# Performance work log

Measured on AMD Instinct MI355X. Metric: run time of the kernel, lower is better.

The kernel has to match this reference:

```python
import jax, jax.numpy as jnp
import numpy as np

# icosphere level-6 mesh dims
B, CIN, COUT = 8, 64, 64
NV_PREV, NV, NF = 10242, 40962, 81920


def spmm(x, rows, cols, vals, nrows):
    # x: [..., ncols]; sparse S [nrows, ncols] in COO -> y[..., r] = sum S[r,c] x[..., c]
    out = jnp.zeros(x.shape[:-1] + (nrows,), x.dtype)
    return out.at[..., rows].add(x[..., cols] * vals)


def setup_inputs() -> dict:
    key = jax.random.key(0)
    ks = jax.random.split(key, 12)
    x = jax.random.normal(ks[0], (B, CIN, NV_PREV), jnp.float32)
    # G: per-face gradient operator [3*NF, NV], 3 nnz per row (face vertices)
    G_rows = jnp.repeat(jnp.arange(3 * NF, dtype=jnp.int32), 3)
    G_cols = jax.random.randint(ks[1], (3 * NF * 3,), 0, NV, dtype=jnp.int32)
    G_vals = jax.random.normal(ks[2], (3 * NF * 3,), jnp.float32) * 0.1
    # L: vertex Laplacian [NV, NV], ~7 nnz per row
    L_rows = jnp.repeat(jnp.arange(NV, dtype=jnp.int32), 7)
    L_cols = jax.random.randint(ks[3], (NV * 7,), 0, NV, dtype=jnp.int32)
    L_vals = jax.random.normal(ks[4], (NV * 7,), jnp.float32) * 0.1
    # F2V: face-to-vertex averaging [NV, NF], ~6 nnz per row
    F2V_rows = jnp.repeat(jnp.arange(NV, dtype=jnp.int32), 6)
    F2V_cols = jax.random.randint(ks[5], (NV * 6,), 0, NF, dtype=jnp.int32)
    F2V_vals = jnp.full((NV * 6,), 1.0 / 6.0, jnp.float32)
    # per-face east-west / north-south tangent weights [NF, 3]
    EW = jax.random.normal(ks[6], (NF, 3), jnp.float32)
    NS = jax.random.normal(ks[7], (NF, 3), jnp.float32)
    # learned parameters
    stdv = 1.0 / np.sqrt(CIN * 4)
    coeffs = jax.random.uniform(ks[8], (COUT, CIN, 4), jnp.float32, -stdv, stdv)
    bias = jax.random.uniform(ks[9], (COUT,), jnp.float32, -stdv, stdv)
    return {
        "x": x,
        "G_rows": G_rows, "G_cols": G_cols, "G_vals": G_vals,
        "L_rows": L_rows, "L_cols": L_cols, "L_vals": L_vals,
        "F2V_rows": F2V_rows, "F2V_cols": F2V_cols, "F2V_vals": F2V_vals,
        "EW": EW, "NS": NS, "coeffs": coeffs, "bias": bias,
    }


def reference(x, G_rows, G_cols, G_vals, L_rows, L_cols, L_vals,
              F2V_rows, F2V_cols, F2V_vals, EW, NS, coeffs, bias):
    b, c = x.shape[:2]
    # pad new (upsampled) vertices with ones: [B, C, NV]
    xin = jnp.concatenate([x, jnp.ones((b, c, NV - NV_PREV), x.dtype)], axis=-1)
    # per-face gradient: [B, C, 3*NF] -> [B, C, NF, 3]
    grad_face = spmm(xin, G_rows, G_cols, G_vals, 3 * NF)
    grad_face = grad_face.reshape(b, c, 3, NF).transpose(0, 1, 3, 2)
    # Laplacian: [B, C, NV]
    laplacian = spmm(xin, L_rows, L_cols, L_vals, NV)
    # project face gradients onto EW/NS tangent dirs: [B, C, NF]
    grad_face_ew = jnp.sum(grad_face * EW, axis=-1)
    grad_face_ns = jnp.sum(grad_face * NS, axis=-1)
    # average back to vertices: [B, C, NV]
    grad_vert_ew = spmm(grad_face_ew, F2V_rows, F2V_cols, F2V_vals, NV)
    grad_vert_ns = spmm(grad_face_ns, F2V_rows, F2V_cols, F2V_vals, NV)
    # fuse 4 feature maps with learned coeffs: [B, CIN, NV, 4] x [COUT, CIN, 4]
    feat = jnp.stack([xin, laplacian, grad_vert_ew, grad_vert_ns], axis=-1)
    out = jnp.einsum("bcvk,ock->bov", feat, coeffs) + bias[:, None]
    return out
```

## Files before the change

kernel.cpp:

```cpp
#include <hip/hip_runtime.h>
#include <hip/hip_bf16.h>

typedef __hip_bfloat16 bf16;
typedef __attribute__((ext_vector_type(8))) short short8;
typedef __attribute__((ext_vector_type(4))) float floatx4;

#define NVP 10242
#define NV  40962
#define NF  81920
#define VPB 32
#define FPW 4

__device__ __forceinline__ float bfbits2f(unsigned short u) {
    union { unsigned int i; float f; } cv; cv.i = ((unsigned int)u) << 16;
    return cv.f;
}
__device__ __forceinline__ unsigned short f2bfbits(float f) {
    bf16 h = __float2bfloat16(f);
    return __builtin_bit_cast(unsigned short, h);
}
__device__ __forceinline__ unsigned short pk_fp8(float a, float b) {
    int p = __builtin_amdgcn_cvt_pk_fp8_f32(a, b, 0, false);
    return (unsigned short)(p & 0xffff);
}
__device__ __forceinline__ unsigned char one_fp8(float a) {
    int p = __builtin_amdgcn_cvt_pk_fp8_f32(a, 0.f, 0, false);
    return (unsigned char)(p & 0xff);
}
__device__ __forceinline__ float fp8_lo(unsigned int u) {
    return __builtin_amdgcn_cvt_f32_fp8(u, 0);
}
__device__ __forceinline__ float fp8_hi(unsigned int u) {
    return __builtin_amdgcn_cvt_f32_fp8(u, 1);
}

__global__ void k_prep(const float* __restrict__ coeffs,
                       unsigned short* __restrict__ coeffsB,
                       const int* __restrict__ G_cols,
                       const float* __restrict__ G_vals,
                       const float* __restrict__ EW,
                       const float* __restrict__ NS,
                       float* __restrict__ Gpk,
                       const int* __restrict__ L_cols,
                       const float* __restrict__ L_vals,
                       const int* __restrict__ F2V_cols,
                       const float* __restrict__ F2V_vals,
                       float* __restrict__ Vpk) {
    int b = blockIdx.x;
    if (b < 64) {
        int t = b * 256 + threadIdx.x;
        int j = t & 7, lane = (t >> 3) & 63, s = t >> 9;
        int ot = s >> 3, kk = s & 7;
        int o  = ot * 16 + (lane & 15);
        int kg = kk * 32 + (lane >> 4) * 8 + j;
        coeffsB[t] = f2bfbits(coeffs[o * 256 + kg]);
    } else if (b < 384) {
        int f = (b - 64) * 256 + threadIdx.x;
        float r[32];
#pragma unroll
        for (int q = 0; q < 32; ++q) r[q] = 0.f;
#pragma unroll
        for (int d = 0; d < 3; ++d)
#pragma unroll
            for (int j = 0; j < 3; ++j) {
                int idx = (d * NF + f) * 3 + j;
                r[d * 3 + j]      = __int_as_float(G_cols[idx]);
                r[16 + d * 3 + j] = G_vals[idx];
            }
#pragma unroll
        for (int d = 0; d < 3; ++d) {
            r[25 + d] = EW[f * 3 + d];
            r[28 + d] = NS[f * 3 + d];
        }
        float4* dst = (float4*)(Gpk + (size_t)f * 32);
#pragma unroll
        for (int q = 0; q < 8; ++q) dst[q] = ((const float4*)r)[q];
    } else {
        int v = (b - 384) * 256 + threadIdx.x;
        if (v >= NV) return;
        float r[32];
#pragma unroll
        for (int q = 0; q < 32; ++q) r[q] = 0.f;
#pragma unroll
        for (int j = 0; j < 7; ++j) {
            r[j]      = __int_as_float(L_cols[v * 7 + j]);
            r[16 + j] = L_vals[v * 7 + j];
        }
#pragma unroll
        for (int j = 0; j < 6; ++j) {
            r[8 + j]  = __int_as_float(F2V_cols[v * 6 + j]);
            r[24 + j] = F2V_vals[v * 6 + j];
        }
        float4* dst = (float4*)(Vpk + (size_t)v * 32);
#pragma unroll
        for (int q = 0; q < 8; ++q) dst[q] = ((const float4*)r)[q];
    }
}

__global__ void k_transpose(const float* __restrict__ x,
                            unsigned short* __restrict__ xin,
                            unsigned char* __restrict__ xin8) {
    x    += (size_t)blockIdx.y * 64 * NVP;
    xin  += (size_t)blockIdx.y * 64 * NV;
    xin8 += (size_t)blockIdx.y * 64 * NV;
    __shared__ float tile[64][65];
    int v0 = blockIdx.x * 64;
    int tx = threadIdx.x & 63;
    int ty = threadIdx.x >> 6;
    int v  = v0 + tx;
#pragma unroll
    for (int r = 0; r < 16; ++r) {
        int c = ty + r * 4;
        tile[tx][c] = (v < NVP) ? x[c * NVP + v] : 1.0f;
    }
    __syncthreads();
#pragma unroll
    for (int r = 0; r < 16; ++r) {
        int vl = ty + r * 4;
        int vv = v0 + vl;
        if (vv < NV) {
            float val = tile[vl][tx];
            xin [vv * 64 + tx] = f2bfbits(val);
            xin8[vv * 64 + tx] = one_fp8(val);
        }
    }
}

__global__ void __launch_bounds__(256, 4) k_facegrad(
    const unsigned char* __restrict__ xin8,
    const float* __restrict__ Gpk,
    unsigned short* __restrict__ gfi, int nbm, int nbs) {
    int batch = blockIdx.x & nbm;
    int fblk  = blockIdx.x >> nbs;
    xin8 += (size_t)batch * 64 * NV;
    gfi  += (size_t)batch * 64 * NF;
    int w  = __builtin_amdgcn_readfirstlane(threadIdx.x >> 6);
    int c  = threadIdx.x & 63;
    int f0 = (fblk * 4 + w) * FPW;

    int gc[FPW][9];
#pragma unroll
    for (int i = 0; i < FPW; ++i) {
        const int* ri = (const int*)(Gpk + (size_t)(f0 + i) * 32);
#pragma unroll
        for (int j = 0; j < 9; ++j) gc[i][j] = ri[j];
    }
    unsigned int xv[FPW][9];
#pragma unroll
    for (int i = 0; i < FPW; ++i)
#pragma unroll
        for (int j = 0; j < 9; ++j)
            xv[i][j] = xin8[(size_t)gc[i][j] * 64 + c];
#pragma unroll
    for (int i = 0; i < FPW; ++i) {
        const float* rf = Gpk + (size_t)(f0 + i) * 32;
        float g0 = rf[16] * fp8_lo(xv[i][0]) + rf[17] * fp8_lo(xv[i][1])
                 + rf[18] * fp8_lo(xv[i][2]);
        float g1 = rf[19] * fp8_lo(xv[i][3]) + rf[20] * fp8_lo(xv[i][4])
                 + rf[21] * fp8_lo(xv[i][5]);
        float g2 = rf[22] * fp8_lo(xv[i][6]) + rf[23] * fp8_lo(xv[i][7])
                 + rf[24] * fp8_lo(xv[i][8]);
        float ew = g0 * rf[25] + g1 * rf[26] + g2 * rf[27];
        float ns = g0 * rf[28] + g1 * rf[29] + g2 * rf[30];
        gfi[(f0 + i) * 64 + c] = pk_fp8(ew, ns);
    }
}

__global__ void __launch_bounds__(512, 2) k_vertex(
    const unsigned short* __restrict__ xin,
    const unsigned char* __restrict__ xin8,
    const float* __restrict__ Vpk,
    const unsigned short* __restrict__ gfi,
    const unsigned short* __restrict__ coeffsB,
    const float* __restrict__ bias,
    float* __restrict__ out,
    int nbm, int nbs) {
    int batch = blockIdx.x & nbm;
    int vb    = (blockIdx.x >> nbs) * VPB;
    xin  += (size_t)batch * 64 * NV;
    xin8 += (size_t)batch * 64 * NV;
    gfi  += (size_t)batch * 64 * NF;
    out  += (size_t)batch * 64 * NV;

    __shared__ unsigned short feat[VPB * 264];
    __shared__ float outs[VPB * 65];
    int w    = __builtin_amdgcn_readfirstlane(threadIdx.x >> 6);
    int lane = threadIdx.x & 63;
    int c    = lane;

    int vcs[4];
#pragma unroll
    for (int i = 0; i < 4; ++i) {
        int v = vb + w * 4 + i;
        vcs[i] = __builtin_amdgcn_readfirstlane(v < NV ? v : NV - 1);
    }
    int lc[4][7], fc[4][6];
#pragma unroll
    for (int i = 0; i < 4; ++i) {
        const int* ri = (const int*)(Vpk + (size_t)vcs[i] * 32);
#pragma unroll
        for (int j = 0; j < 7; ++j) lc[i][j] = ri[j];
#pragma unroll
        for (int j = 0; j < 6; ++j) fc[i][j] = ri[8 + j];
    }
    unsigned int f0u[4], xl[4][7], gg[4][6];
#pragma unroll
    for (int i = 0; i < 4; ++i) {
        f0u[i] = xin[(size_t)vcs[i] * 64 + c];
#pragma unroll
        for (int j = 0; j < 7; ++j)
            xl[i][j] = xin8[(size_t)lc[i][j] * 64 + c];
#pragma unroll
        for (int j = 0; j < 6; ++j)
            gg[i][j] = gfi[(size_t)fc[i][j] * 64 + c];
    }
#pragma unroll
    for (int i = 0; i < 4; ++i) {
        const float* rv = Vpk + (size_t)vcs[i] * 32;
        float lap = 0.f;
#pragma unroll
        for (int j = 0; j < 7; ++j)
            lap += rv[16 + j] * fp8_lo(xl[i][j]);
        float ew = 0.f, ns = 0.f;
#pragma unroll
        for (int j = 0; j < 6; ++j) {
            float val = rv[24 + j];
            ew += val * fp8_lo(gg[i][j]);
            ns += val * fp8_hi(gg[i][j]);
        }
        ushort4 p = make_ushort4((unsigned short)f0u[i], f2bfbits(lap),
                                 f2bfbits(ew), f2bfbits(ns));
        *(ushort4*)&feat[(w * 4 + i) * 264 + c * 4] = p;
    }
    __syncthreads();

    int m = lane & 15, quad = lane >> 4;
    int ot = w & 3, vh = w >> 2;
    float bo = bias[ot * 16 + m];
    floatx4 acc = {bo, bo, bo, bo};
#pragma unroll
    for (int kk = 0; kk < 8; ++kk) {
        short8 a = *(const short8*)&feat[(vh * 16 + m) * 264 + kk * 32 + quad * 8];
        short8 bfr = *(const short8*)&coeffsB[((ot * 8 + kk) * 64 + lane) * 8];
        acc = __builtin_amdgcn_mfma_f32_16x16x32_bf16(a, bfr, acc, 0, 0, 0);
    }

#pragma unroll
    for (int r = 0; r < 4; ++r)
        outs[(vh * 16 + quad * 4 + r) * 65 + ot * 16 + m] = acc[r];
    __syncthreads();
    int vp = threadIdx.x & 31;
    int og = threadIdx.x >> 5;
    if (vb + vp < NV) {
#pragma unroll
        for (int r = 0; r < 4; ++r) {
            int o2 = og + r * 16;
            out[(size_t)o2 * NV + vb + vp] = outs[vp * 65 + o2];
        }
    }
}

extern "C" void kernel_launch(void* const* d_in, const int* in_sizes, int n_in,
                              void* d_out, int out_size, void* d_ws, size_t ws_size,
                              hipStream_t stream) {
    const float* x        = (const float*)d_in[0];
    const int*   G_cols   = (const int*)  d_in[2];
    const float* G_vals   = (const float*)d_in[3];
    const int*   L_cols   = (const int*)  d_in[5];
    const float* L_vals   = (const float*)d_in[6];
    const int*   F2V_cols = (const int*)  d_in[8];
    const float* F2V_vals = (const float*)d_in[9];
    const float* EW       = (const float*)d_in[10];
    const float* NS       = (const float*)d_in[11];
    const float* coeffs   = (const float*)d_in[12];
    const float* bias     = (const float*)d_in[13];
    float* out = (float*)d_out;

    char* ws = (char*)d_ws;
    const size_t xin_b = (size_t)NV * 64;
    const size_t gf_b  = (size_t)NF * 64;
    const size_t gpk_bytes = (size_t)NF * 128;
    const size_t vpk_bytes = (size_t)NV * 128;
    const size_t fixed = 65536 + gpk_bytes + vpk_bytes;
    size_t perb = 2 * xin_b + 2 * gf_b + xin_b;
    int nb = (ws_size >= fixed + 8 * perb) ? 8
           : (ws_size >= fixed + 2 * perb) ? 2 : 1;
    int nbs = (nb == 8) ? 3 : (nb == 2) ? 1 : 0;

    unsigned short* coeffsB = (unsigned short*)ws;
    float* Gpk = (float*)(ws + 65536);
    float* Vpk = Gpk + (size_t)NF * 32;
    unsigned short* xin  = (unsigned short*)(ws + fixed);
    unsigned short* gfi  = xin + (size_t)nb * xin_b;
    unsigned char*  xin8 = (unsigned char*)(gfi + (size_t)nb * gf_b);

    k_prep<<<545, 256, 0, stream>>>(coeffs, coeffsB, G_cols, G_vals, EW, NS,
                                    Gpk, L_cols, L_vals, F2V_cols, F2V_vals,
                                    Vpk);
    const int nvb = (NV + VPB - 1) / VPB;
    const int nfb = NF / (4 * FPW);
    for (int b0 = 0; b0 < 8; b0 += nb) {
        dim3 gt(641, nb);
        k_transpose<<<gt, 256, 0, stream>>>(x + (size_t)b0 * 64 * NVP, xin, xin8);
        k_facegrad<<<nfb * nb, 256, 0, stream>>>(xin8, Gpk, gfi, nb - 1, nbs);
        k_vertex<<<nvb * nb, 512, 0, stream>>>(xin, xin8, Vpk, gfi, coeffsB,
                                               bias, out + (size_t)b0 * 64 * NV,
                                               nb - 1, nbs);
    }
}
```

Measured before the change: 308.4 us.

## Interleave all batches per vertex so each gather fetches eight batches at once

Intermediate buffers are re-laid out so that, for every vertex or face and channel, the values of all 8 batches sit next to each other (8 fp8 bytes, 8 bf16 values, or 8 packed gradient pairs). Each indexed gather in the face-gradient and vertex kernels then loads a 64-bit or 128-bit word covering all batches, so index lookups and scattered memory transactions are shared across the batch. The vertex kernel now handles one vertex per wave across 8 batches, and the batch loop and the workspace-size fallback are removed. In exchange it always needs the full 8-batch workspace, holds more registers per thread, and the output store writes 8-float runs per row, which coalesces less well.

```diff
diff --git a/kernel.cpp b/kernel.cpp
--- a/kernel.cpp
+++ b/kernel.cpp
@@ -4,17 +4,13 @@
 typedef __hip_bfloat16 bf16;
 typedef __attribute__((ext_vector_type(8))) short short8;
 typedef __attribute__((ext_vector_type(4))) float floatx4;
+typedef unsigned long long u64;
 
 #define NVP 10242
 #define NV  40962
 #define NF  81920
-#define VPB 32
-#define FPW 4
-
-__device__ __forceinline__ float bfbits2f(unsigned short u) {
-    union { unsigned int i; float f; } cv; cv.i = ((unsigned int)u) << 16;
-    return cv.f;
-}
+#define FPF 2
+
 __device__ __forceinline__ unsigned short f2bfbits(float f) {
     bf16 h = __float2bfloat16(f);
     return __builtin_bit_cast(unsigned short, h);
@@ -27,11 +23,14 @@
     int p = __builtin_amdgcn_cvt_pk_fp8_f32(a, 0.f, 0, false);
     return (unsigned char)(p & 0xff);
 }
-__device__ __forceinline__ float fp8_lo(unsigned int u) {
-    return __builtin_amdgcn_cvt_f32_fp8(u, 0);
-}
-__device__ __forceinline__ float fp8_hi(unsigned int u) {
-    return __builtin_amdgcn_cvt_f32_fp8(u, 1);
+__device__ __forceinline__ float f8s0(unsigned int u){return __builtin_amdgcn_cvt_f32_fp8(u,0);}
+__device__ __forceinline__ float f8s1(unsigned int u){return __builtin_amdgcn_cvt_f32_fp8(u,1);}
+__device__ __forceinline__ float f8s2(unsigned int u){return __builtin_amdgcn_cvt_f32_fp8(u,2);}
+__device__ __forceinline__ float f8s3(unsigned int u){return __builtin_amdgcn_cvt_f32_fp8(u,3);}
+__device__ __forceinline__ void unpack8(u64 v, float o[8]) {
+    unsigned int lo = (unsigned int)v, hi = (unsigned int)(v >> 32);
+    o[0]=f8s0(lo); o[1]=f8s1(lo); o[2]=f8s2(lo); o[3]=f8s3(lo);
+    o[4]=f8s0(hi); o[5]=f8s1(hi); o[6]=f8s2(hi); o[7]=f8s3(hi);
 }
 
 __global__ void k_prep(const float* __restrict__ coeffs,
@@ -97,165 +96,197 @@
     }
 }
 
-__global__ void k_transpose(const float* __restrict__ x,
-                            unsigned short* __restrict__ xin,
-                            unsigned char* __restrict__ xin8) {
-    x    += (size_t)blockIdx.y * 64 * NVP;
-    xin  += (size_t)blockIdx.y * 64 * NV;
-    xin8 += (size_t)blockIdx.y * 64 * NV;
-    __shared__ float tile[64][65];
+__global__ void __launch_bounds__(256) k_transpose(
+    const float* __restrict__ x,
+    uint4* __restrict__ xinp, u64* __restrict__ xin8p) {
+    __shared__ u64 t8 [32][65];
+    __shared__ u64 tbL[32][65];
+    __shared__ u64 tbH[32][65];
     int v0 = blockIdx.x * 64;
-    int tx = threadIdx.x & 63;
-    int ty = threadIdx.x >> 6;
-    int v  = v0 + tx;
-#pragma unroll
-    for (int r = 0; r < 16; ++r) {
-        int c = ty + r * 4;
-        tile[tx][c] = (v < NVP) ? x[c * NVP + v] : 1.0f;
-    }
-    __syncthreads();
-#pragma unroll
-    for (int r = 0; r < 16; ++r) {
-        int vl = ty + r * 4;
-        int vv = v0 + vl;
-        if (vv < NV) {
-            float val = tile[vl][tx];
-            xin [vv * 64 + tx] = f2bfbits(val);
-            xin8[vv * 64 + tx] = one_fp8(val);
+    int tx = threadIdx.x & 63, ty = threadIdx.x >> 6;
+    for (int half = 0; half < 2; ++half) {
+        if (half) __syncthreads();
+#pragma unroll
+        for (int r = 0; r < 8; ++r) {
+            int c  = ty + r * 4;
+            int cg = half * 32 + c;
+            int v  = v0 + tx;
+            u64 p8 = 0, bL = 0, bH = 0;
+#pragma unroll
+            for (int b = 0; b < 8; ++b) {
+                float val = (v < NVP) ? x[((size_t)b * 64 + cg) * NVP + v] : 1.0f;
+                p8 |= (u64)one_fp8(val) << (8 * b);
+                u64 bf = (u64)f2bfbits(val);
+                if (b < 4) bL |= bf << (16 * b);
+                else       bH |= bf << (16 * (b - 4));
+            }
+            t8[c][tx] = p8; tbL[c][tx] = bL; tbH[c][tx] = bH;
+        }
+        __syncthreads();
+        int cc = threadIdx.x & 31;
+        int vq = threadIdx.x >> 5;
+#pragma unroll
+        for (int it = 0; it < 8; ++it) {
+            int v  = vq * 8 + it;
+            int vg = v0 + v;
+            if (vg < NV) {
+                size_t idx = (size_t)vg * 64 + half * 32 + cc;
+                xin8p[idx] = t8[cc][v];
+                u64 lo = tbL[cc][v], hi = tbH[cc][v];
+                xinp[idx] = make_uint4((unsigned)lo, (unsigned)(lo >> 32),
+                                       (unsigned)hi, (unsigned)(hi >> 32));
+            }
         }
     }
 }
 
 __global__ void __launch_bounds__(256, 4) k_facegrad(
-    const unsigned char* __restrict__ xin8,
+    const u64* __restrict__ xin8p,
     const float* __restrict__ Gpk,
-    unsigned short* __restrict__ gfi, int nbm, int nbs) {
-    int batch = blockIdx.x & nbm;
-    int fblk  = blockIdx.x >> nbs;
-    xin8 += (size_t)batch * 64 * NV;
-    gfi  += (size_t)batch * 64 * NF;
+    uint4* __restrict__ gfip) {
     int w  = __builtin_amdgcn_readfirstlane(threadIdx.x >> 6);
     int c  = threadIdx.x & 63;
-    int f0 = (fblk * 4 + w) * FPW;
-
-    int gc[FPW][9];
-#pragma unroll
-    for (int i = 0; i < FPW; ++i) {
+    int f0 = (blockIdx.x * 4 + w) * FPF;
+
+    int gc[FPF][9];
+#pragma unroll
+    for (int i = 0; i < FPF; ++i) {
         const int* ri = (const int*)(Gpk + (size_t)(f0 + i) * 32);
 #pragma unroll
         for (int j = 0; j < 9; ++j) gc[i][j] = ri[j];
     }
-    unsigned int xv[FPW][9];
-#pragma unroll
-    for (int i = 0; i < FPW; ++i)
+    u64 xv[FPF][9];
+#pragma unroll
+    for (int i = 0; i < FPF; ++i)
 #pragma unroll
         for (int j = 0; j < 9; ++j)
-            xv[i][j] = xin8[(size_t)gc[i][j] * 64 + c];
-#pragma unroll
-    for (int i = 0; i < FPW; ++i) {
+            xv[i][j] = xin8p[(size_t)gc[i][j] * 64 + c];
+    __builtin_amdgcn_sched_barrier(0);
+#pragma unroll
+    for (int i = 0; i < FPF; ++i) {
         const float* rf = Gpk + (size_t)(f0 + i) * 32;
-        float g0 = rf[16] * fp8_lo(xv[i][0]) + rf[17] * fp8_lo(xv[i][1])
-                 + rf[18] * fp8_lo(xv[i][2]);
-        float g1 = rf[19] * fp8_lo(xv[i][3]) + rf[20] * fp8_lo(xv[i][4])
-                 + rf[21] * fp8_lo(xv[i][5]);
-        float g2 = rf[22] * fp8_lo(xv[i][6]) + rf[23] * fp8_lo(xv[i][7])
-                 + rf[24] * fp8_lo(xv[i][8]);
-        float ew = g0 * rf[25] + g1 * rf[26] + g2 * rf[27];
-        float ns = g0 * rf[28] + g1 * rf[29] + g2 * rf[30];
-        gfi[(f0 + i) * 64 + c] = pk_fp8(ew, ns);
+        float g0[8], g1[8], g2[8];
+#pragma unroll
+        for (int b = 0; b < 8; ++b) { g0[b] = 0.f; g1[b] = 0.f; g2[b] = 0.f; }
+#pragma unroll
+        for (int j = 0; j < 3; ++j) {
+            float fa[8], fb[8], fc_[8];
+            unpack8(xv[i][j],     fa);
+            unpack8(xv[i][3 + j], fb);
+            unpack8(xv[i][6 + j], fc_);
+            float va = rf[16 + j], vb = rf[19 + j], vc = rf[22 + j];
+#pragma unroll
+            for (int b = 0; b < 8; ++b) {
+                g0[b] += va * fa[b];
+                g1[b] += vb * fb[b];
+                g2[b] += vc * fc_[b];
+            }
+        }
+        float e0 = rf[25], e1 = rf[26], e2 = rf[27];
+        float n0 = rf[28], n1 = rf[29], n2 = rf[30];
+        unsigned int d[4] = {0u, 0u, 0u, 0u};
+#pragma unroll
+        for (int b = 0; b < 8; ++b) {
+            float ew = g0[b] * e0 + g1[b] * e1 + g2[b] * e2;
+            float ns = g0[b] * n0 + g1[b] * n1 + g2[b] * n2;
+            d[b >> 1] |= (unsigned int)pk_fp8(ew, ns) << ((b & 1) * 16);
+        }
+        gfip[(size_t)(f0 + i) * 64 + c] = make_uint4(d[0], d[1], d[2], d[3]);
     }
 }
 
 __global__ void __launch_bounds__(512, 2) k_vertex(
-    const unsigned short* __restrict__ xin,
-    const unsigned char* __restrict__ xin8,
+    const uint4* __restrict__ xinp,
+    const u64* __restrict__ xin8p,
     const float* __restrict__ Vpk,
-    const unsigned short* __restrict__ gfi,
+    const uint4* __restrict__ gfip,
     const unsigned short* __restrict__ coeffsB,
     const float* __restrict__ bias,
-    float* __restrict__ out,
-    int nbm, int nbs) {
-    int batch = blockIdx.x & nbm;
-    int vb    = (blockIdx.x >> nbs) * VPB;
-    xin  += (size_t)batch * 64 * NV;
-    xin8 += (size_t)batch * 64 * NV;
-    gfi  += (size_t)batch * 64 * NF;
-    out  += (size_t)batch * 64 * NV;
-
-    __shared__ unsigned short feat[VPB * 264];
-    __shared__ float outs[VPB * 65];
+    float* __restrict__ out) {
+    int vb = blockIdx.x * 8;
+    __shared__ unsigned short feat[64 * 264];
+    __shared__ float outs[64 * 67];
     int w    = __builtin_amdgcn_readfirstlane(threadIdx.x >> 6);
-    int lane = threadIdx.x & 63;
-    int c    = lane;
-
-    int vcs[4];
-#pragma unroll
-    for (int i = 0; i < 4; ++i) {
-        int v = vb + w * 4 + i;
-        vcs[i] = __builtin_amdgcn_readfirstlane(v < NV ? v : NV - 1);
-    }
-    int lc[4][7], fc[4][6];
-#pragma unroll
-    for (int i = 0; i < 4; ++i) {
-        const int* ri = (const int*)(Vpk + (size_t)vcs[i] * 32);
-#pragma unroll
-        for (int j = 0; j < 7; ++j) lc[i][j] = ri[j];
-#pragma unroll
-        for (int j = 0; j < 6; ++j) fc[i][j] = ri[8 + j];
-    }
-    unsigned int f0u[4], xl[4][7], gg[4][6];
-#pragma unroll
-    for (int i = 0; i < 4; ++i) {
-        f0u[i] = xin[(size_t)vcs[i] * 64 + c];
-#pragma unroll
-        for (int j = 0; j < 7; ++j)
-            xl[i][j] = xin8[(size_t)lc[i][j] * 64 + c];
-#pragma unroll
-        for (int j = 0; j < 6; ++j)
-            gg[i][j] = gfi[(size_t)fc[i][j] * 64 + c];
-    }
-#pragma unroll
-    for (int i = 0; i < 4; ++i) {
-        const float* rv = Vpk + (size_t)vcs[i] * 32;
-        float lap = 0.f;
-#pragma unroll
-        for (int j = 0; j < 7; ++j)
-            lap += rv[16 + j] * fp8_lo(xl[i][j]);
-        float ew = 0.f, ns = 0.f;
-#pragma unroll
-        for (int j = 0; j < 6; ++j) {
-            float val = rv[24 + j];
-            ew += val * fp8_lo(gg[i][j]);
-            ns += val * fp8_hi(gg[i][j]);
-        }
-        ushort4 p = make_ushort4((unsigned short)f0u[i], f2bfbits(lap),
-                                 f2bfbits(ew), f2bfbits(ns));
-        *(ushort4*)&feat[(w * 4 + i) * 264 + c * 4] = p;
+    int c    = threadIdx.x & 63;
+    int v    = vb + w;
+    int vcs  = __builtin_amdgcn_readfirstlane(v < NV ? v : NV - 1);
+
+    const int* ri = (const int*)(Vpk + (size_t)vcs * 32);
+    int lc[7], fc[6];
+#pragma unroll
+    for (int j = 0; j < 7; ++j) lc[j] = ri[j];
+#pragma unroll
+    for (int j = 0; j < 6; ++j) fc[j] = ri[8 + j];
+    uint4 f0q = xinp[(size_t)vcs * 64 + c];
+    u64 xl[7];
+#pragma unroll
+    for (int j = 0; j < 7; ++j) xl[j] = xin8p[(size_t)lc[j] * 64 + c];
+    uint4 gq[6];
+#pragma unroll
+    for (int j = 0; j < 6; ++j) gq[j] = gfip[(size_t)fc[j] * 64 + c];
+    __builtin_amdgcn_sched_barrier(0);
+    const float* rv = Vpk + (size_t)vcs * 32;
+    float lap[8], ew[8], ns[8];
+#pragma unroll
+    for (int b = 0; b < 8; ++b) { lap[b] = 0.f; ew[b] = 0.f; ns[b] = 0.f; }
+#pragma unroll
+    for (int j = 0; j < 7; ++j) {
+        float xa[8];
+        unpack8(xl[j], xa);
+        float lv = rv[16 + j];
+#pragma unroll
+        for (int b = 0; b < 8; ++b) lap[b] += lv * xa[b];
+    }
+#pragma unroll
+    for (int j = 0; j < 6; ++j) {
+        float val = rv[24 + j];
+        unsigned int q0 = gq[j].x, q1 = gq[j].y, q2 = gq[j].z, q3 = gq[j].w;
+        ew[0] += val * f8s0(q0); ns[0] += val * f8s1(q0);
+        ew[1] += val * f8s2(q0); ns[1] += val * f8s3(q0);
+        ew[2] += val * f8s0(q1); ns[2] += val * f8s1(q1);
+        ew[3] += val * f8s2(q1); ns[3] += val * f8s3(q1);
+        ew[4] += val * f8s0(q2); ns[4] += val * f8s1(q2);
+        ew[5] += val * f8s2(q2); ns[5] += val * f8s3(q2);
+        ew[6] += val * f8s0(q3); ns[6] += val * f8s1(q3);
+        ew[7] += val * f8s2(q3); ns[7] += val * f8s3(q3);
+    }
+    unsigned int fd[4] = {f0q.x, f0q.y, f0q.z, f0q.w};
+#pragma unroll
+    for (int b = 0; b < 8; ++b) {
+        unsigned short f0s = (unsigned short)(fd[b >> 1] >> ((b & 1) * 16));
+        ushort4 p = make_ushort4(f0s, f2bfbits(lap[b]),
+                                 f2bfbits(ew[b]), f2bfbits(ns[b]));
+        *(ushort4*)&feat[(w * 8 + b) * 264 + c * 4] = p;
     }
     __syncthreads();
 
-    int m = lane & 15, quad = lane >> 4;
-    int ot = w & 3, vh = w >> 2;
-    float bo = bias[ot * 16 + m];
-    floatx4 acc = {bo, bo, bo, bo};
+    int m = c & 15, quad = c >> 4;
+    int rt = w & 3, ob = (w >> 2) * 2;
+    float b0v = bias[ob * 16 + m], b1v = bias[(ob + 1) * 16 + m];
+    floatx4 acc0 = {b0v, b0v, b0v, b0v};
+    floatx4 acc1 = {b1v, b1v, b1v, b1v};
 #pragma unroll
     for (int kk = 0; kk < 8; ++kk) {
-        short8 a = *(const short8*)&feat[(vh * 16 + m) * 264 + kk * 32 + quad * 8];
-        short8 bfr = *(const short8*)&coeffsB[((ot * 8 + kk) * 64 + lane) * 8];
-        acc = __builtin_amdgcn_mfma_f32_16x16x32_bf16(a, bfr, acc, 0, 0, 0);
-    }
-
-#pragma unroll
-    for (int r = 0; r < 4; ++r)
-        outs[(vh * 16 + quad * 4 + r) * 65 + ot * 16 + m] = acc[r];
+        short8 a  = *(const short8*)&feat[(rt * 16 + m) * 264 + kk * 32 + quad * 8];
+        short8 f0 = *(const short8*)&coeffsB[((ob * 8 + kk) * 64 + c) * 8];
+        short8 f1 = *(const short8*)&coeffsB[(((ob + 1) * 8 + kk) * 64 + c) * 8];
+        acc0 = __builtin_amdgcn_mfma_f32_16x16x32_bf16(a, f0, acc0, 0, 0, 0);
+        acc1 = __builtin_amdgcn_mfma_f32_16x16x32_bf16(a, f1, acc1, 0, 0, 0);
+    }
+#pragma unroll
+    for (int r = 0; r < 4; ++r) {
+        outs[(rt * 16 + quad * 4 + r) * 67 + ob * 16 + m]       = acc0[r];
+        outs[(rt * 16 + quad * 4 + r) * 67 + (ob + 1) * 16 + m] = acc1[r];
+    }
     __syncthreads();
-    int vp = threadIdx.x & 31;
-    int og = threadIdx.x >> 5;
-    if (vb + vp < NV) {
-#pragma unroll
-        for (int r = 0; r < 4; ++r) {
-            int o2 = og + r * 16;
-            out[(size_t)o2 * NV + vb + vp] = outs[vp * 65 + o2];
+
+    int vloc = threadIdx.x & 7;
+    int g    = threadIdx.x >> 3;
+    if (vb + vloc < NV) {
+#pragma unroll
+        for (int p = 0; p < 8; ++p) {
+            out[((size_t)p * 64 + g) * NV + vb + vloc] =
+                outs[(vloc * 8 + p) * 67 + g];
         }
     }
 }
@@ -277,34 +308,24 @@
     float* out = (float*)d_out;
 
     char* ws = (char*)d_ws;
-    const size_t xin_b = (size_t)NV * 64;
-    const size_t gf_b  = (size_t)NF * 64;
-    const size_t gpk_bytes = (size_t)NF * 128;
-    const size_t vpk_bytes = (size_t)NV * 128;
-    const size_t fixed = 65536 + gpk_bytes + vpk_bytes;
-    size_t perb = 2 * xin_b + 2 * gf_b + xin_b;
-    int nb = (ws_size >= fixed + 8 * perb) ? 8
-           : (ws_size >= fixed + 2 * perb) ? 2 : 1;
-    int nbs = (nb == 8) ? 3 : (nb == 2) ? 1 : 0;
+    const size_t gpk_bytes  = (size_t)NF * 128;
+    const size_t vpk_bytes  = (size_t)NV * 128;
+    const size_t xinp_bytes = (size_t)NV * 64 * 16;
+    const size_t x8p_bytes  = (size_t)NV * 64 * 8;
 
     unsigned short* coeffsB = (unsigned short*)ws;
-    float* Gpk = (float*)(ws + 65536);
-    float* Vpk = Gpk + (size_t)NF * 32;
-    unsigned short* xin  = (unsigned short*)(ws + fixed);
-    unsigned short* gfi  = xin + (size_t)nb * xin_b;
-    unsigned char*  xin8 = (unsigned char*)(gfi + (size_t)nb * gf_b);
+    float* Gpk   = (float*)(ws + 65536);
+    float* Vpk   = (float*)(ws + 65536 + gpk_bytes);
+    uint4* xinp  = (uint4*)(ws + 65536 + gpk_bytes + vpk_bytes);
+    u64*   xin8p = (u64*)  (ws + 65536 + gpk_bytes + vpk_bytes + xinp_bytes);
+    uint4* gfip  = (uint4*)(ws + 65536 + gpk_bytes + vpk_bytes + xinp_bytes
+                               + x8p_bytes);
 
     k_prep<<<545, 256, 0, stream>>>(coeffs, coeffsB, G_cols, G_vals, EW, NS,
                                     Gpk, L_cols, L_vals, F2V_cols, F2V_vals,
                                     Vpk);
-    const int nvb = (NV + VPB - 1) / VPB;
-    const int nfb = NF / (4 * FPW);
-    for (int b0 = 0; b0 < 8; b0 += nb) {
-        dim3 gt(641, nb);
-        k_transpose<<<gt, 256, 0, stream>>>(x + (size_t)b0 * 64 * NVP, xin, xin8);
-        k_facegrad<<<nfb * nb, 256, 0, stream>>>(xin8, Gpk, gfi, nb - 1, nbs);
-        k_vertex<<<nvb * nb, 512, 0, stream>>>(xin, xin8, Vpk, gfi, coeffsB,
-                                               bias, out + (size_t)b0 * 64 * NV,
-                                               nb - 1, nbs);
-    }
-}
+    k_transpose<<<641, 256, 0, stream>>>(x, xinp, xin8p);
+    k_facegrad<<<NF / (4 * FPF), 256, 0, stream>>>(xin8p, Gpk, gfip);
+    k_vertex<<<(NV + 7) / 8, 512, 0, stream>>>(xinp, xin8p, Vpk, gfip,
+                                               coeffsB, bias, out);
+}
```

Result: slower. 331.5 us (+7.5%).

## Fuse prep and transpose, drop batch chunking, shrink vertex pack, split vertex kernel

Applied to the files above, without the earlier changes.

Merges the transpose and the prep kernel into one launch, always processes all 8 batches at once (the workspace-size fallback is gone), and packs the vertex metadata into 28 floats instead of 32. Scheduling barriers are added so the gathers issue before the math, and the vertex pass is split into two launches, one of which forces its gathered registers to stay live. This cuts launch count and metadata traffic, but assumes the workspace is always large enough and adds an extra kernel launch for the vertex stage.

```diff
diff --git a/kernel.cpp b/kernel.cpp
--- a/kernel.cpp
+++ b/kernel.cpp
@@ -4,17 +4,16 @@
 typedef __hip_bfloat16 bf16;
 typedef __attribute__((ext_vector_type(8))) short short8;
 typedef __attribute__((ext_vector_type(4))) float floatx4;
+typedef unsigned long long u64;
 
 #define NVP 10242
 #define NV  40962
 #define NF  81920
 #define VPB 32
 #define FPW 4
-
-__device__ __forceinline__ float bfbits2f(unsigned short u) {
-    union { unsigned int i; float f; } cv; cv.i = ((unsigned int)u) << 16;
-    return cv.f;
-}
+#define NVB 1281
+#define TBLK 5128
+
 __device__ __forceinline__ unsigned short f2bfbits(float f) {
     bf16 h = __float2bfloat16(f);
     return __builtin_bit_cast(unsigned short, h);
@@ -27,26 +26,55 @@
     int p = __builtin_amdgcn_cvt_pk_fp8_f32(a, 0.f, 0, false);
     return (unsigned char)(p & 0xff);
 }
-__device__ __forceinline__ float fp8_lo(unsigned int u) {
-    return __builtin_amdgcn_cvt_f32_fp8(u, 0);
-}
-__device__ __forceinline__ float fp8_hi(unsigned int u) {
-    return __builtin_amdgcn_cvt_f32_fp8(u, 1);
-}
-
-__global__ void k_prep(const float* __restrict__ coeffs,
-                       unsigned short* __restrict__ coeffsB,
-                       const int* __restrict__ G_cols,
-                       const float* __restrict__ G_vals,
-                       const float* __restrict__ EW,
-                       const float* __restrict__ NS,
-                       float* __restrict__ Gpk,
-                       const int* __restrict__ L_cols,
-                       const float* __restrict__ L_vals,
-                       const int* __restrict__ F2V_cols,
-                       const float* __restrict__ F2V_vals,
-                       float* __restrict__ Vpk) {
-    int b = blockIdx.x;
+__device__ __forceinline__ float f8s0(unsigned int u){return __builtin_amdgcn_cvt_f32_fp8(u,0);}
+__device__ __forceinline__ float f8s1(unsigned int u){return __builtin_amdgcn_cvt_f32_fp8(u,1);}
+
+__global__ void __launch_bounds__(256) k_pt(
+    const float* __restrict__ x,
+    unsigned short* __restrict__ xin,
+    unsigned char* __restrict__ xin8,
+    const float* __restrict__ coeffs,
+    unsigned short* __restrict__ coeffsB,
+    const int* __restrict__ G_cols,
+    const float* __restrict__ G_vals,
+    const float* __restrict__ EW,
+    const float* __restrict__ NS,
+    float* __restrict__ Gpk,
+    const int* __restrict__ L_cols,
+    const float* __restrict__ L_vals,
+    const int* __restrict__ F2V_cols,
+    const float* __restrict__ F2V_vals,
+    float* __restrict__ Vpk) {
+    __shared__ float tile[64][65];
+    int bid = blockIdx.x;
+    if (bid < TBLK) {
+        int batch = bid & 7;
+        int v0    = (bid >> 3) * 64;
+        const float* xb = x + (size_t)batch * 64 * NVP;
+        unsigned short* xinb  = xin  + (size_t)batch * NV * 64;
+        unsigned char*  xin8b = xin8 + (size_t)batch * NV * 64;
+        int tx = threadIdx.x & 63;
+        int ty = threadIdx.x >> 6;
+        int v  = v0 + tx;
+#pragma unroll
+        for (int r = 0; r < 16; ++r) {
+            int c = ty + r * 4;
+            tile[tx][c] = (v < NVP) ? xb[c * NVP + v] : 1.0f;
+        }
+        __syncthreads();
+#pragma unroll
+        for (int r = 0; r < 16; ++r) {
+            int vl = ty + r * 4;
+            int vv = v0 + vl;
+            if (vv < NV) {
+                float val = tile[vl][tx];
+                xinb [vv * 64 + tx] = f2bfbits(val);
+                xin8b[vv * 64 + tx] = one_fp8(val);
+            }
+        }
+        return;
+    }
+    int b = bid - TBLK;
     if (b < 64) {
         int t = b * 256 + threadIdx.x;
         int j = t & 7, lane = (t >> 3) & 63, s = t >> 9;
@@ -78,60 +106,31 @@
     } else {
         int v = (b - 384) * 256 + threadIdx.x;
         if (v >= NV) return;
-        float r[32];
-#pragma unroll
-        for (int q = 0; q < 32; ++q) r[q] = 0.f;
+        float r[28];
+#pragma unroll
+        for (int q = 0; q < 28; ++q) r[q] = 0.f;
 #pragma unroll
         for (int j = 0; j < 7; ++j) {
             r[j]      = __int_as_float(L_cols[v * 7 + j]);
-            r[16 + j] = L_vals[v * 7 + j];
+            r[14 + j] = L_vals[v * 7 + j];
         }
 #pragma unroll
         for (int j = 0; j < 6; ++j) {
-            r[8 + j]  = __int_as_float(F2V_cols[v * 6 + j]);
-            r[24 + j] = F2V_vals[v * 6 + j];
-        }
-        float4* dst = (float4*)(Vpk + (size_t)v * 32);
-#pragma unroll
-        for (int q = 0; q < 8; ++q) dst[q] = ((const float4*)r)[q];
-    }
-}
-
-__global__ void k_transpose(const float* __restrict__ x,
-                            unsigned short* __restrict__ xin,
-                            unsigned char* __restrict__ xin8) {
-    x    += (size_t)blockIdx.y * 64 * NVP;
-    xin  += (size_t)blockIdx.y * 64 * NV;
-    xin8 += (size_t)blockIdx.y * 64 * NV;
-    __shared__ float tile[64][65];
-    int v0 = blockIdx.x * 64;
-    int tx = threadIdx.x & 63;
-    int ty = threadIdx.x >> 6;
-    int v  = v0 + tx;
-#pragma unroll
-    for (int r = 0; r < 16; ++r) {
-        int c = ty + r * 4;
-        tile[tx][c] = (v < NVP) ? x[c * NVP + v] : 1.0f;
-    }
-    __syncthreads();
-#pragma unroll
-    for (int r = 0; r < 16; ++r) {
-        int vl = ty + r * 4;
-        int vv = v0 + vl;
-        if (vv < NV) {
-            float val = tile[vl][tx];
-            xin [vv * 64 + tx] = f2bfbits(val);
-            xin8[vv * 64 + tx] = one_fp8(val);
-        }
+            r[7 + j]  = __int_as_float(F2V_cols[v * 6 + j]);
+            r[21 + j] = F2V_vals[v * 6 + j];
+        }
+        float4* dst = (float4*)(Vpk + (size_t)v * 28);
+#pragma unroll
+        for (int q = 0; q < 7; ++q) dst[q] = ((const float4*)r)[q];
     }
 }
 
 __global__ void __launch_bounds__(256, 4) k_facegrad(
     const unsigned char* __restrict__ xin8,
     const float* __restrict__ Gpk,
-    unsigned short* __restrict__ gfi, int nbm, int nbs) {
-    int batch = blockIdx.x & nbm;
-    int fblk  = blockIdx.x >> nbs;
+    unsigned short* __restrict__ gfi) {
+    int batch = blockIdx.x & 7;
+    int fblk  = blockIdx.x >> 3;
     xin8 += (size_t)batch * 64 * NV;
     gfi  += (size_t)batch * 64 * NF;
     int w  = __builtin_amdgcn_readfirstlane(threadIdx.x >> 6);
@@ -151,32 +150,34 @@
 #pragma unroll
         for (int j = 0; j < 9; ++j)
             xv[i][j] = xin8[(size_t)gc[i][j] * 64 + c];
+    __builtin_amdgcn_sched_barrier(0);
 #pragma unroll
     for (int i = 0; i < FPW; ++i) {
         const float* rf = Gpk + (size_t)(f0 + i) * 32;
-        float g0 = rf[16] * fp8_lo(xv[i][0]) + rf[17] * fp8_lo(xv[i][1])
-                 + rf[18] * fp8_lo(xv[i][2]);
-        float g1 = rf[19] * fp8_lo(xv[i][3]) + rf[20] * fp8_lo(xv[i][4])
-                 + rf[21] * fp8_lo(xv[i][5]);
-        float g2 = rf[22] * fp8_lo(xv[i][6]) + rf[23] * fp8_lo(xv[i][7])
-                 + rf[24] * fp8_lo(xv[i][8]);
+        float g0 = rf[16] * f8s0(xv[i][0]) + rf[17] * f8s0(xv[i][1])
+                 + rf[18] * f8s0(xv[i][2]);
+        float g1 = rf[19] * f8s0(xv[i][3]) + rf[20] * f8s0(xv[i][4])
+                 + rf[21] * f8s0(xv[i][5]);
+        float g2 = rf[22] * f8s0(xv[i][6]) + rf[23] * f8s0(xv[i][7])
+                 + rf[24] * f8s0(xv[i][8]);
         float ew = g0 * rf[25] + g1 * rf[26] + g2 * rf[27];
         float ns = g0 * rf[28] + g1 * rf[29] + g2 * rf[30];
         gfi[(f0 + i) * 64 + c] = pk_fp8(ew, ns);
     }
 }
 
-__global__ void __launch_bounds__(512, 2) k_vertex(
+template <int KEEP_ALIVE>
+__device__ __forceinline__ void vertex_body(
     const unsigned short* __restrict__ xin,
     const unsigned char* __restrict__ xin8,
     const float* __restrict__ Vpk,
     const unsigned short* __restrict__ gfi,
     const unsigned short* __restrict__ coeffsB,
     const float* __restrict__ bias,
-    float* __restrict__ out,
-    int nbm, int nbs) {
-    int batch = blockIdx.x & nbm;
-    int vb    = (blockIdx.x >> nbs) * VPB;
+    float* __restrict__ out, int vbBase) {
+    int batch = blockIdx.x & 7;
+    int vbIdx = vbBase + (blockIdx.x >> 3);
+    int vb    = vbIdx * VPB;
     xin  += (size_t)batch * 64 * NV;
     xin8 += (size_t)batch * 64 * NV;
     gfi  += (size_t)batch * 64 * NF;
@@ -197,11 +198,11 @@
     int lc[4][7], fc[4][6];
 #pragma unroll
     for (int i = 0; i < 4; ++i) {
-        const int* ri = (const int*)(Vpk + (size_t)vcs[i] * 32);
+        const int* ri = (const int*)(Vpk + (size_t)vcs[i] * 28);
 #pragma unroll
         for (int j = 0; j < 7; ++j) lc[i][j] = ri[j];
 #pragma unroll
-        for (int j = 0; j < 6; ++j) fc[i][j] = ri[8 + j];
+        for (int j = 0; j < 6; ++j) fc[i][j] = ri[7 + j];
     }
     unsigned int f0u[4], xl[4][7], gg[4][6];
 #pragma unroll
@@ -214,19 +215,31 @@
         for (int j = 0; j < 6; ++j)
             gg[i][j] = gfi[(size_t)fc[i][j] * 64 + c];
     }
+    __builtin_amdgcn_sched_barrier(0);
+    if (KEEP_ALIVE) {
+#pragma unroll
+        for (int i = 0; i < 4; ++i) {
+            asm volatile("" :: "v"(f0u[i]));
+#pragma unroll
+            for (int j = 0; j < 7; ++j) asm volatile("" :: "v"(xl[i][j]));
+#pragma unroll
+            for (int j = 0; j < 6; ++j) asm volatile("" :: "v"(gg[i][j]));
+        }
+        __builtin_amdgcn_sched_barrier(0);
+    }
 #pragma unroll
     for (int i = 0; i < 4; ++i) {
-        const float* rv = Vpk + (size_t)vcs[i] * 32;
+        const float* rv = Vpk + (size_t)vcs[i] * 28;
         float lap = 0.f;
 #pragma unroll
         for (int j = 0; j < 7; ++j)
-            lap += rv[16 + j] * fp8_lo(xl[i][j]);
+            lap += rv[14 + j] * f8s0(xl[i][j]);
         float ew = 0.f, ns = 0.f;
 #pragma unroll
         for (int j = 0; j < 6; ++j) {
-            float val = rv[24 + j];
-            ew += val * fp8_lo(gg[i][j]);
-            ns += val * fp8_hi(gg[i][j]);
+            float val = rv[21 + j];
+            ew += val * f8s0(gg[i][j]);
+            ns += val * f8s1(gg[i][j]);
         }
         ushort4 p = make_ushort4((unsigned short)f0u[i], f2bfbits(lap),
                                  f2bfbits(ew), f2bfbits(ns));
@@ -246,18 +259,40 @@
     }
 
 #pragma unroll
-    for (int r = 0; r < 4; ++r)
-        outs[(vh * 16 + quad * 4 + r) * 65 + ot * 16 + m] = acc[r];
+    for (int r2 = 0; r2 < 4; ++r2)
+        outs[(vh * 16 + quad * 4 + r2) * 65 + ot * 16 + m] = acc[r2];
     __syncthreads();
     int vp = threadIdx.x & 31;
     int og = threadIdx.x >> 5;
     if (vb + vp < NV) {
 #pragma unroll
-        for (int r = 0; r < 4; ++r) {
-            int o2 = og + r * 16;
+        for (int r2 = 0; r2 < 4; ++r2) {
+            int o2 = og + r2 * 16;
             out[(size_t)o2 * NV + vb + vp] = outs[vp * 65 + o2];
         }
     }
+}
+
+__global__ void __launch_bounds__(512, 2) k_vertex_a(
+    const unsigned short* __restrict__ xin,
+    const unsigned char* __restrict__ xin8,
+    const float* __restrict__ Vpk,
+    const unsigned short* __restrict__ gfi,
+    const unsigned short* __restrict__ coeffsB,
+    const float* __restrict__ bias,
+    float* __restrict__ out, int vbBase) {
+    vertex_body<0>(xin, xin8, Vpk, gfi, coeffsB, bias, out, vbBase);
+}
+
+__global__ void __launch_bounds__(512, 2) k_vertex_b(
+    const unsigned short* __restrict__ xin,
+    const unsigned char* __restrict__ xin8,
+    const float* __restrict__ Vpk,
+    const unsigned short* __restrict__ gfi,
+    const unsigned short* __restrict__ coeffsB,
+    const float* __restrict__ bias,
+    float* __restrict__ out, int vbBase) {
+    vertex_body<1>(xin, xin8, Vpk, gfi, coeffsB, bias, out, vbBase);
 }
 
 extern "C" void kernel_launch(void* const* d_in, const int* in_sizes, int n_in,
@@ -277,34 +312,25 @@
     float* out = (float*)d_out;
 
     char* ws = (char*)d_ws;
-    const size_t xin_b = (size_t)NV * 64;
-    const size_t gf_b  = (size_t)NF * 64;
     const size_t gpk_bytes = (size_t)NF * 128;
-    const size_t vpk_bytes = (size_t)NV * 128;
-    const size_t fixed = 65536 + gpk_bytes + vpk_bytes;
-    size_t perb = 2 * xin_b + 2 * gf_b + xin_b;
-    int nb = (ws_size >= fixed + 8 * perb) ? 8
-           : (ws_size >= fixed + 2 * perb) ? 2 : 1;
-    int nbs = (nb == 8) ? 3 : (nb == 2) ? 1 : 0;
+    const size_t vpk_bytes = (size_t)NV * 112;
+    const size_t xin_bytes = (size_t)8 * NV * 64 * 2;
+    const size_t x8_bytes  = (size_t)8 * NV * 64;
 
     unsigned short* coeffsB = (unsigned short*)ws;
     float* Gpk = (float*)(ws + 65536);
-    float* Vpk = Gpk + (size_t)NF * 32;
-    unsigned short* xin  = (unsigned short*)(ws + fixed);
-    unsigned short* gfi  = xin + (size_t)nb * xin_b;
-    unsigned char*  xin8 = (unsigned char*)(gfi + (size_t)nb * gf_b);
-
-    k_prep<<<545, 256, 0, stream>>>(coeffs, coeffsB, G_cols, G_vals, EW, NS,
-                                    Gpk, L_cols, L_vals, F2V_cols, F2V_vals,
-                                    Vpk);
-    const int nvb = (NV + VPB - 1) / VPB;
-    const int nfb = NF / (4 * FPW);
-    for (int b0 = 0; b0 < 8; b0 += nb) {
-        dim3 gt(641, nb);
-        k_transpose<<<gt, 256, 0, stream>>>(x + (size_t)b0 * 64 * NVP, xin, xin8);
-        k_facegrad<<<nfb * nb, 256, 0, stream>>>(xin8, Gpk, gfi, nb - 1, nbs);
-        k_vertex<<<nvb * nb, 512, 0, stream>>>(xin, xin8, Vpk, gfi, coeffsB,
-                                               bias, out + (size_t)b0 * 64 * NV,
-                                               nb - 1, nbs);
-    }
-}
+    float* Vpk = (float*)(ws + 65536 + gpk_bytes);
+    unsigned short* xin  = (unsigned short*)(ws + 65536 + gpk_bytes + vpk_bytes);
+    unsigned char*  xin8 = (unsigned char*)((char*)xin + xin_bytes);
+    unsigned short* gfi  = (unsigned short*)((char*)xin8 + x8_bytes);
+
+    k_pt<<<TBLK + 545, 256, 0, stream>>>(x, xin, xin8,
+                                         coeffs, coeffsB, G_cols, G_vals,
+                                         EW, NS, Gpk, L_cols, L_vals,
+                                         F2V_cols, F2V_vals, Vpk);
+    k_facegrad<<<(NF / (4 * FPW)) * 8, 256, 0, stream>>>(xin8, Gpk, gfi);
+    k_vertex_a<<<641 * 8, 512, 0, stream>>>(xin, xin8, Vpk, gfi, coeffsB,
+                                            bias, out, 0);
+    k_vertex_b<<<640 * 8, 512, 0, stream>>>(xin, xin8, Vpk, gfi, coeffsB,
+                                            bias, out, 641);
+}
```

Result: slower. 342.5 us (+11.1%).
